# Optimization experiments

Measured on AMD Instinct MI355X. Metric: run time of the kernel, lower is better.

The kernel has to match this reference:

```python
import jax, jax.numpy as jnp
import numpy as np

N, D, RDIM, R, L = 512, 768, 100, 8, 2
EPS = 1e-5


def _ln(x, g, b):
    m = jnp.mean(x, axis=-1, keepdims=True)
    v = jnp.var(x, axis=-1, keepdims=True)
    return (x - m) * jax.lax.rsqrt(v + EPS) * g + b


def _conv2d(x, w, b):
    y = jax.lax.conv_general_dilated(x, w, (1, 1), 'SAME',
                                     dimension_numbers=('NCHW', 'OIHW', 'NCHW'))
    return y + b[None, :, None, None]


def setup_inputs() -> dict:
    key = jax.random.key(0)
    ks = jax.random.split(key, 10)
    s = 0.02
    inv = 1.0 / np.sqrt(D).astype(np.float32)
    return {
        'ents': jax.random.normal(ks[0], (N, D), jnp.float32),
        'R_local': jax.random.normal(ks[1], (L, RDIM, D, D), jnp.float32) * inv,
        'rel_mlp_w': jax.random.normal(ks[2], (R, RDIM), jnp.float32) * s,
        'rel_mlp_b': jnp.zeros((R,), jnp.float32),
        'conv1_w': jax.random.normal(ks[3], (L, 2 * RDIM, RDIM, 3, 3), jnp.float32) * s,
        'conv1_b': jnp.zeros((L, 2 * RDIM), jnp.float32),
        'conv2_w': jax.random.normal(ks[4], (L, RDIM, 2 * RDIM, 3, 3), jnp.float32) * s,
        'conv2_b': jnp.zeros((L, RDIM), jnp.float32),
        'posffn_ln_g': jnp.ones((L, RDIM), jnp.float32),
        'posffn_ln_b': jnp.zeros((L, RDIM), jnp.float32),
        'rel_ln_g': jnp.ones((L, RDIM), jnp.float32),
        'rel_ln_b': jnp.zeros((L, RDIM), jnp.float32),
        'mh_wf': jax.random.normal(ks[5], (L, R, D, D // R), jnp.float32) * inv,
        'mh_wb': jax.random.normal(ks[6], (L, R, D, D // R), jnp.float32) * inv,
        'mh_b': jnp.zeros((L, R, D // R), jnp.float32),
        'ent_mlp_w': jax.random.normal(ks[7], (L, D, D), jnp.float32) * inv,
        'ent_mlp_b': jnp.zeros((L, D), jnp.float32),
        'ent_ln_g': jnp.ones((L, D), jnp.float32),
        'ent_ln_b': jnp.zeros((L, D), jnp.float32),
    }


def reference(ents, R_local, rel_mlp_w, rel_mlp_b, conv1_w, conv1_b, conv2_w, conv2_b,
              posffn_ln_g, posffn_ln_b, rel_ln_g, rel_ln_b, mh_wf, mh_wb, mh_b,
              ent_mlp_w, ent_mlp_b, ent_ln_g, ent_ln_b):
    # Eval mode: dropout and dropedge are identity.
    prev_rels = None
    I = jnp.eye(N, dtype=ents.dtype)
    for l in range(L):
        residual = ents
        # ReRescal: rel[i, j, r] = e_i^T R_r e_j, then ReLU  -> [N, N, RDIM]
        t = jnp.einsum('id,rde->ire', ents, R_local[l])
        rel_embs = jax.nn.relu(jnp.einsum('ire,je->ijr', t, ents))
        if prev_rels is not None:
            rel_embs = _ln(rel_embs + prev_rels, rel_ln_g[l], rel_ln_b[l])
        # posFFN2d: 3x3 conv FFN over the NxN relation grid + residual layernorm
        res = rel_embs
        h = rel_embs.transpose(2, 0, 1)[None]  # [1, RDIM, N, N]
        h = jax.nn.relu(_conv2d(h, conv1_w[l], conv1_b[l]))
        h = _conv2d(h, conv2_w[l], conv2_b[l])[0].transpose(1, 2, 0)
        rel_embs = _ln(h + res, posffn_ln_g[l], posffn_ln_b[l])
        # relation logits -> softmax over relation axis -> [R, N, N] adjacency
        iap = jnp.einsum('ijd,rd->rij', rel_embs, rel_mlp_w) + rel_mlp_b[:, None, None]
        A = jax.nn.softmax(iap, axis=0)
        # Laplace smoothing: D^-1/2 (A + I) D^-1/2
        A_hat = A + I[None]
        dis = jax.lax.rsqrt(jnp.sum(A_hat, axis=2))
        dis = jnp.where(jnp.isinf(dis), 0.0, dis)
        A = dis[:, :, None] * A_hat * dis[:, None, :]
        # multi-head directed GCN (single layer, arch=[])
        hf = jnp.einsum('nd,rdo->rno', ents, mh_wf[l])
        hb = jnp.einsum('nd,rdo->rno', ents, mh_wb[l])
        out = (jnp.einsum('rmn,rno->rmo', A, hf)
               + jnp.einsum('rnm,rno->rmo', A, hb)
               + mh_b[l][:, None, :])
        out = jax.nn.relu(out)  # [R, N, D//R]
        e = out.transpose(1, 0, 2).reshape(N, D)
        # ent_mlp (single Linear) + residual layernorm
        e = jnp.einsum('nd,od->no', e, ent_mlp_w[l]) + ent_mlp_b[l]
        ents = _ln(e + residual, ent_ln_g[l], ent_ln_b[l])
        prev_rels = rel_embs
    rels = jnp.einsum('ijd,rd->ijr', prev_rels, rel_mlp_w) + rel_mlp_b
    return (ents, rels)
```

## Files before the change

kernel.cpp:

```cpp
#include <hip/hip_runtime.h>
#include <hip/hip_bf16.h>


static constexpr long NNpix = 512L * 512L;

typedef __attribute__((ext_vector_type(8))) short short8v;
typedef __attribute__((ext_vector_type(4))) float f32x4;

__device__ inline float bf2f(short s) {
    unsigned u = ((unsigned)(unsigned short)s) << 16;
    float f; __builtin_memcpy(&f, &u, 4);
    return f;
}
__device__ inline short f2bf(float f) {
    unsigned u; __builtin_memcpy(&u, &f, 4);
    u += 0x7fff + ((u >> 16) & 1);
    return (short)(u >> 16);
}
__device__ inline void gload_lds16(const short* g, short* l) {
    __builtin_amdgcn_global_load_lds(
        (const __attribute__((address_space(1))) unsigned int*)g,
        (__attribute__((address_space(3))) unsigned int*)l, 16, 0, 0);
}

template <bool RELU>
__global__ __launch_bounds__(256) void bgemm_xyt(
    const short* __restrict__ X, long sX,
    const short* __restrict__ Y, long sY,
    short* __restrict__ D, long sD,
    int M, int N, int K)
{
    X += (long)blockIdx.z * sX;
    Y += (long)blockIdx.z * sY;
    D += (long)blockIdx.z * sD;

    __shared__ short Xs[128 * 32];
    __shared__ short Ys[128 * 32];

    const int tid = threadIdx.x, wv = tid >> 6, ln = tid & 63;
    const int wr = wv >> 1, wc = wv & 1;
    const int m0 = blockIdx.y * 128, n0 = blockIdx.x * 128;

    f32x4 acc[4][4] = {};

    const int srow = ln >> 2;
    const int sk8 = ln & 3;
    const int fr = ln & 15, fk = (ln >> 4) * 8;

    for (int k0 = 0; k0 < K; k0 += 32) {
#pragma unroll
        for (int i = wv; i < 8; i += 4) {
            gload_lds16(X + (long)(m0 + i * 16 + srow) * K + k0 + sk8 * 8,
                        Xs + i * 512);
            gload_lds16(Y + (long)(n0 + i * 16 + srow) * K + k0 + sk8 * 8,
                        Ys + i * 512);
        }
        __syncthreads();
        short8v a[4], b[4];
#pragma unroll
        for (int mi = 0; mi < 4; ++mi)
            a[mi] = *(const short8v*)(Xs + (wr * 64 + mi * 16 + fr) * 32 + fk);
#pragma unroll
        for (int ni = 0; ni < 4; ++ni)
            b[ni] = *(const short8v*)(Ys + (wc * 64 + ni * 16 + fr) * 32 + fk);
#pragma unroll
        for (int mi = 0; mi < 4; ++mi)
#pragma unroll
            for (int ni = 0; ni < 4; ++ni)
                acc[mi][ni] = __builtin_amdgcn_mfma_f32_16x16x32_bf16(
                    a[mi], b[ni], acc[mi][ni], 0, 0, 0);
        __syncthreads();
    }

    const int fv = (ln >> 4) * 4;
#pragma unroll
    for (int mi = 0; mi < 4; ++mi)
#pragma unroll
        for (int ni = 0; ni < 4; ++ni)
#pragma unroll
            for (int v = 0; v < 4; ++v) {
                const int row = m0 + wr * 64 + mi * 16 + fv + v;
                const int col = n0 + wc * 64 + ni * 16 + fr;
                float x = acc[mi][ni][v];
                if (RELU) x = fmaxf(x, 0.f);
                D[(long)row * N + col] = f2bf(x);
            }
}

__global__ __launch_bounds__(256) void bgemm_bias_f32(
    const short* __restrict__ X,
    const short* __restrict__ Y,
    float* __restrict__ D,
    const float* __restrict__ bias,
    int M, int N, int K)
{
    __shared__ short Xs[128 * 32];
    __shared__ short Ys[128 * 32];

    const int tid = threadIdx.x, wv = tid >> 6, ln = tid & 63;
    const int wr = wv >> 1, wc = wv & 1;
    const int m0 = blockIdx.y * 128, n0 = blockIdx.x * 128;

    f32x4 acc[4][4] = {};

    const int srow = ln >> 2;
    const int sk8 = ln & 3;
    const int fr = ln & 15, fk = (ln >> 4) * 8;

    for (int k0 = 0; k0 < K; k0 += 32) {
#pragma unroll
        for (int i = wv; i < 8; i += 4) {
            gload_lds16(X + (long)(m0 + i * 16 + srow) * K + k0 + sk8 * 8,
                        Xs + i * 512);
            gload_lds16(Y + (long)(n0 + i * 16 + srow) * K + k0 + sk8 * 8,
                        Ys + i * 512);
        }
        __syncthreads();
        short8v a[4], b[4];
#pragma unroll
        for (int mi = 0; mi < 4; ++mi)
            a[mi] = *(const short8v*)(Xs + (wr * 64 + mi * 16 + fr) * 32 + fk);
#pragma unroll
        for (int ni = 0; ni < 4; ++ni)
            b[ni] = *(const short8v*)(Ys + (wc * 64 + ni * 16 + fr) * 32 + fk);
#pragma unroll
        for (int mi = 0; mi < 4; ++mi)
#pragma unroll
            for (int ni = 0; ni < 4; ++ni)
                acc[mi][ni] = __builtin_amdgcn_mfma_f32_16x16x32_bf16(
                    a[mi], b[ni], acc[mi][ni], 0, 0, 0);
        __syncthreads();
    }

    const int fv = (ln >> 4) * 4;
#pragma unroll
    for (int mi = 0; mi < 4; ++mi)
#pragma unroll
        for (int ni = 0; ni < 4; ++ni)
#pragma unroll
            for (int v = 0; v < 4; ++v) {
                const int row = m0 + wr * 64 + mi * 16 + fv + v;
                const int col = n0 + wc * 64 + ni * 16 + fr;
                D[(long)row * N + col] = acc[mi][ni][v] + bias[col];
            }
}

template <int CINP, int CINW, int COUT, int OUTP, bool RELU>
__global__ __launch_bounds__(256) void conv_gemm(
    const short* __restrict__ img,
    const short* __restrict__ wflat,
    const float* __restrict__ bias,
    short* __restrict__ out)
{
    constexpr int NCH = CINW / 32;
    constexpr int KW = 9 * CINW;

    __shared__ short Xs[144 * 32];
    __shared__ short Ys[3 * 128 * 32];

    const int tid = threadIdx.x, wv = tid >> 6, ln = tid & 63;
    const int wr = wv >> 1, wc = wv & 1;
    const int bx = blockIdx.x;
    const int bsw = (bx & 7) * ((int)gridDim.x >> 3) + (bx >> 3);
    const int m0 = bsw * 128;
    const int n0 = blockIdx.y * 128;

    f32x4 acc[4][4] = {};

    const int srow = ln >> 2;
    const int sk8 = ln & 3;
    const int fr = ln & 15, fk = (ln >> 4) * 8;

    for (int ky = 0; ky < 3; ++ky) {
        const int slab0 = m0 + (ky - 1) * 512 - 1;
        for (int cc = 0; cc < NCH; ++cc) {
            const int ci0 = cc * 32;
#pragma unroll
            for (int i = wv; i < 9; i += 4) {
                int rpx = slab0 + i * 16 + srow;
                rpx = rpx < 0 ? 0 : (rpx > (int)NNpix - 1 ? (int)NNpix - 1 : rpx);
                gload_lds16(img + (long)rpx * CINP + ci0 + sk8 * 8,
                            Xs + i * 512);
            }
#pragma unroll
            for (int kx = 0; kx < 3; ++kx) {
                const int wbase = (ky * 3 + kx) * CINW;
#pragma unroll
                for (int i = wv; i < 8; i += 4)
                    gload_lds16(wflat + (long)(n0 + i * 16 + srow) * KW + wbase + ci0 + sk8 * 8,
                                Ys + kx * 4096 + i * 512);
            }
            __syncthreads();
#pragma unroll
            for (int kx = 0; kx < 3; ++kx) {
                short8v a[4], b[4];
#pragma unroll
                for (int mi = 0; mi < 4; ++mi)
                    a[mi] = *(const short8v*)(Xs + (wr * 64 + mi * 16 + fr + kx) * 32 + fk);
#pragma unroll
                for (int ni = 0; ni < 4; ++ni)
                    b[ni] = *(const short8v*)(Ys + kx * 4096 + (wc * 64 + ni * 16 + fr) * 32 + fk);
#pragma unroll
                for (int mi = 0; mi < 4; ++mi)
#pragma unroll
                    for (int ni = 0; ni < 4; ++ni)
                        acc[mi][ni] = __builtin_amdgcn_mfma_f32_16x16x32_bf16(
                            a[mi], b[ni], acc[mi][ni], 0, 0, 0);
            }
            __syncthreads();
        }
    }

    const int fv = (ln >> 4) * 4;
#pragma unroll
    for (int mi = 0; mi < 4; ++mi)
#pragma unroll
        for (int ni = 0; ni < 4; ++ni)
#pragma unroll
            for (int v = 0; v < 4; ++v) {
                const int px = m0 + wr * 64 + mi * 16 + fv + v;
                const int co = n0 + wc * 64 + ni * 16 + fr;
                if (co < COUT) {
                    float x = acc[mi][ni][v] + bias[co];
                    if (RELU) x = fmaxf(x, 0.f);
                    out[(long)px * OUTP + co] = f2bf(x);
                } else if (co < OUTP) {
                    out[(long)px * OUTP + co] = 0;
                }
            }
}

template <int CINP, int CINW>
__global__ __launch_bounds__(256) void edge_gather(
    const short* __restrict__ img, short* __restrict__ EP)
{
    constexpr int KW = 9 * CINW;
    const int e = blockIdx.x;
    int y, x;
    bool real = true;
    if (e < 512)       { y = 0;   x = e; }
    else if (e < 1024) { y = 511; x = e - 512; }
    else if (e < 1534) { x = 0;   y = 1 + (e - 1024); }
    else if (e < 2044) { x = 511; y = 1 + (e - 1534); }
    else               { y = 0; x = 0; real = false; }

    const int tid = threadIdx.x;
    for (int idx = tid; idx < KW / 8; idx += 256) {
        const int tap = idx / (CINW / 8);
        const int c = (idx - tap * (CINW / 8)) * 8;
        short8v v = {0, 0, 0, 0, 0, 0, 0, 0};
        if (real && c < CINP) {
            const int yy = y + tap / 3 - 1, xx = x + tap % 3 - 1;
            if ((unsigned)yy < 512u && (unsigned)xx < 512u)
                v = *(const short8v*)(img + ((long)yy * 512 + xx) * CINP + c);
        }
        *(short8v*)(EP + (long)e * KW + idx * 8) = v;
    }
}

template <int COUT, int OUTP, bool RELU>
__global__ __launch_bounds__(256) void conv_edge_gemm(
    const short* __restrict__ EP,
    const short* __restrict__ wflat,
    const float* __restrict__ bias,
    short* __restrict__ out, int K)
{
    __shared__ short Xs[128 * 32];
    __shared__ short Ys[128 * 32];

    const int tid = threadIdx.x, wv = tid >> 6, ln = tid & 63;
    const int wr = wv >> 1, wc = wv & 1;
    const int m0 = blockIdx.x * 128, n0 = blockIdx.y * 128;

    f32x4 acc[4][4] = {};

    const int srow = ln >> 2;
    const int sk8 = ln & 3;
    const int fr = ln & 15, fk = (ln >> 4) * 8;

    for (int k0 = 0; k0 < K; k0 += 32) {
#pragma unroll
        for (int i = wv; i < 8; i += 4) {
            gload_lds16(EP + (long)(m0 + i * 16 + srow) * K + k0 + sk8 * 8,
                        Xs + i * 512);
            gload_lds16(wflat + (long)(n0 + i * 16 + srow) * K + k0 + sk8 * 8,
                        Ys + i * 512);
        }
        __syncthreads();
        short8v a[4], b[4];
#pragma unroll
        for (int mi = 0; mi < 4; ++mi)
            a[mi] = *(const short8v*)(Xs + (wr * 64 + mi * 16 + fr) * 32 + fk);
#pragma unroll
        for (int ni = 0; ni < 4; ++ni)
            b[ni] = *(const short8v*)(Ys + (wc * 64 + ni * 16 + fr) * 32 + fk);
#pragma unroll
        for (int mi = 0; mi < 4; ++mi)
#pragma unroll
            for (int ni = 0; ni < 4; ++ni)
                acc[mi][ni] = __builtin_amdgcn_mfma_f32_16x16x32_bf16(
                    a[mi], b[ni], acc[mi][ni], 0, 0, 0);
        __syncthreads();
    }

    const int fv = (ln >> 4) * 4;
#pragma unroll
    for (int mi = 0; mi < 4; ++mi)
#pragma unroll
        for (int ni = 0; ni < 4; ++ni)
#pragma unroll
            for (int v = 0; v < 4; ++v) {
                const int e = m0 + wr * 64 + mi * 16 + fv + v;
                const int co = n0 + wc * 64 + ni * 16 + fr;
                if (e >= 2044 || co >= COUT) continue;
                int y, x;
                if (e < 512)       { y = 0;   x = e; }
                else if (e < 1024) { y = 511; x = e - 512; }
                else if (e < 1534) { x = 0;   y = 1 + (e - 1024); }
                else               { x = 511; y = 1 + (e - 1534); }
                float v2 = acc[mi][ni][v] + bias[co];
                if (RELU) v2 = fmaxf(v2, 0.f);
                out[((long)y * 512 + x) * OUTP + co] = f2bf(v2);
            }
}

__global__ __launch_bounds__(256) void r_transpose(
    const float* __restrict__ R, short* __restrict__ Rt)
{
    __shared__ float Ts[64][65];
    const int tid = threadIdx.x;
    const long base = (long)blockIdx.z * 589824;
    const int d0 = blockIdx.y * 64, e0 = blockIdx.x * 64;
    const int c = tid & 63, rbase = tid >> 6;
#pragma unroll
    for (int j = 0; j < 16; ++j) {
        const int r = rbase + j * 4;
        Ts[r][c] = R[base + (long)(d0 + r) * 768 + e0 + c];
    }
    __syncthreads();
#pragma unroll
    for (int j = 0; j < 16; ++j) {
        const int e = rbase + j * 4;
        Rt[base + (long)(e0 + e) * 768 + d0 + c] = f2bf(Ts[c][e]);
    }
}

__global__ __launch_bounds__(256) void wfb_transpose(
    const float* __restrict__ wf, const float* __restrict__ wb,
    short* __restrict__ dst)
{
    __shared__ float Ts[64][65];
    const int tid = threadIdx.x;
    const int z = blockIdx.z;
    const float* src = (z < 8) ? wf + (long)z * 73728 : wb + (long)(z - 8) * 73728;
    const int d0 = blockIdx.x * 64, o0 = blockIdx.y * 64;
    const int c = tid & 63, rbase = tid >> 6;
#pragma unroll
    for (int j = 0; j < 16; ++j) {
        const int r = rbase + j * 4;
        Ts[r][c] = (o0 + c < 96) ? src[(long)(d0 + r) * 96 + o0 + c] : 0.f;
    }
    __syncthreads();
#pragma unroll
    for (int j = 0; j < 16; ++j) {
        const int e = rbase + j * 4;
        dst[(long)z * 98304 + (long)(o0 + e) * 768 + d0 + c] = f2bf(Ts[c][e]);
    }
}

__global__ __launch_bounds__(256) void a_laplace_t(
    const float* __restrict__ Ahat, const float* __restrict__ psum,
    short* __restrict__ ABF, short* __restrict__ ABFT)
{
    __shared__ float Ts[64][65];
    const int tid = threadIdx.x;
    const int r8 = blockIdx.z;
    const long ra = (long)r8 * 262144;
    const int i0 = blockIdx.y * 64, j0 = blockIdx.x * 64;
    const int c = tid & 63, rbase = tid >> 6;
    const float sj = psum[r8 * 1024 + (j0 + c) * 2] + psum[r8 * 1024 + (j0 + c) * 2 + 1];
    const float dj = rsqrtf(sj);
#pragma unroll
    for (int j = 0; j < 16; ++j) {
        const int r = rbase + j * 4;
        const float si = psum[r8 * 1024 + (i0 + r) * 2] + psum[r8 * 1024 + (i0 + r) * 2 + 1];
        const float di = rsqrtf(si);
        const float v = Ahat[ra + (long)(i0 + r) * 512 + j0 + c] * di * dj;
        Ts[r][c] = v;
        ABF[ra + (long)(i0 + r) * 512 + j0 + c] = f2bf(v);
    }
    __syncthreads();
#pragma unroll
    for (int j = 0; j < 16; ++j) {
        const int e = rbase + j * 4;
        ABFT[ra + (long)(j0 + e) * 512 + i0 + c] = f2bf(Ts[c][e]);
    }
}

__global__ __launch_bounds__(256) void gcn_combine(
    const short* __restrict__ O1, const short* __restrict__ O2,
    const float* __restrict__ mhb, short* __restrict__ e)
{
    const int idx = blockIdx.x * 256 + threadIdx.x;
    const int m = idx / 768, c = idx - m * 768;
    const int r = c / 96, o = c - r * 96;
    const long oi = (long)r * 65536 + (long)m * 128 + o;
    float v = bf2f(O1[oi]) + bf2f(O2[oi]) + mhb[c];
    e[idx] = f2bf(fmaxf(v, 0.f));
}

__global__ __launch_bounds__(256) void rel_transpose(
    const short* __restrict__ relc, short* __restrict__ relp)
{
    __shared__ short Ts[64][40];
    const int tid = threadIdx.x;
    const long p0 = (long)blockIdx.x * 64;
    const int r0 = blockIdx.y * 32;
    {
        const int ch = tid >> 3, pxo = (tid & 7) * 8;
        short8v v = {0, 0, 0, 0, 0, 0, 0, 0};
        if (r0 + ch < 100)
            v = *(const short8v*)(relc + (long)(r0 + ch) * NNpix + p0 + pxo);
#pragma unroll
        for (int j = 0; j < 8; ++j) Ts[pxo + j][ch] = v[j];
    }
    __syncthreads();
    const int px = tid >> 2, k8 = (tid & 3) * 8;
    if (r0 + k8 < 112) {
        const short8v o = *(const short8v*)(&Ts[px][k8]);
        *(short8v*)(relp + (p0 + px) * 112 + r0 + k8) = o;
    }
}

__global__ __launch_bounds__(256) void conv_w_flat(
    const float* __restrict__ src, short* __restrict__ dst,
    int COUT, int CIN, int COUTP, int CINW)
{
    const int idx = blockIdx.x * 256 + threadIdx.x;
    const int KW = 9 * CINW;
    const int total = COUTP * KW;
    if (idx >= total) return;
    const int co = idx / KW;
    const int rem = idx - co * KW;
    const int tap = rem / CINW, ci = rem - tap * CINW;
    short v = 0;
    if (co < COUT && ci < CIN)
        v = f2bf(src[((long)co * CIN + ci) * 9 + tap]);
    dst[idx] = v;
}

__global__ __launch_bounds__(256) void f32_to_bf16k(
    const float* __restrict__ src, short* __restrict__ dst, long n)
{
    const long i = (long)blockIdx.x * 256 + threadIdx.x;
    if (i < n) dst[i] = f2bf(src[i]);
}

__global__ __launch_bounds__(256) void ln_pix(
    const short* __restrict__ x, const short* __restrict__ res,
    const float* __restrict__ g, const float* __restrict__ b,
    short* __restrict__ out)
{
    __shared__ float gs[100], bs[100];
    const int tid = threadIdx.x;
    if (tid < 100) { gs[tid] = g[tid]; bs[tid] = b[tid]; }
    __syncthreads();
    const long p = (long)blockIdx.x * 256 + tid;
    const short* xr = x + p * 112;
    const short* rr = res + p * 112;
    float v[104];
    float s = 0.f, ss = 0.f;
#pragma unroll
    for (int q = 0; q < 13; ++q) {
        const short8v xa = *(const short8v*)(xr + q * 8);
        const short8v ra = *(const short8v*)(rr + q * 8);
#pragma unroll
        for (int j = 0; j < 8; ++j) {
            const int idx = q * 8 + j;
            const float t = bf2f(xa[j]) + bf2f(ra[j]);
            if (idx < 100) { v[idx] = t; s += t; ss += t * t; }
        }
    }
    const float mean = s * 0.01f;
    const float var = ss * 0.01f - mean * mean;
    const float inv = rsqrtf(var + 1e-5f);
    short* orow = out + p * 112;
#pragma unroll
    for (int q = 0; q < 14; ++q) {
        short8v o;
#pragma unroll
        for (int j = 0; j < 8; ++j) {
            const int idx = q * 8 + j;
            o[j] = (idx < 100) ? f2bf((v[idx] - mean) * inv * gs[idx] + bs[idx])
                               : (short)0;
        }
        *(short8v*)(orow + q * 8) = o;
    }
}

__global__ __launch_bounds__(256) void rel_softmax_laplace(
    const short* __restrict__ relp,
    const float* __restrict__ w,
    const float* __restrict__ bvec,
    float* __restrict__ Ahat,
    float* __restrict__ psum)
{
    __shared__ float ws[800];
    __shared__ float wred[8][4];
    const int tid = threadIdx.x;
    for (int i = tid; i < 800; i += 256) ws[i] = w[i];
    __syncthreads();

    const int i = blockIdx.y;
    const int j = blockIdx.x * 256 + tid;
    const long p = (long)i * 512 + j;
    const short* row = relp + p * 112;

    float acc[8];
#pragma unroll
    for (int r8 = 0; r8 < 8; ++r8) acc[r8] = bvec[r8];
#pragma unroll
    for (int q = 0; q < 13; ++q) {
        const short8v v = *(const short8v*)(row + q * 8);
#pragma unroll
        for (int jj = 0; jj < 8; ++jj) {
            const int r = q * 8 + jj;
            if (r < 100) {
                const float x = bf2f(v[jj]);
#pragma unroll
                for (int r8 = 0; r8 < 8; ++r8)
                    acc[r8] = fmaf(x, ws[r8 * 100 + r], acc[r8]);
            }
        }
    }
    float m = acc[0];
#pragma unroll
    for (int r8 = 1; r8 < 8; ++r8) m = fmaxf(m, acc[r8]);
    float s = 0.f;
#pragma unroll
    for (int r8 = 0; r8 < 8; ++r8) { acc[r8] = expf(acc[r8] - m); s += acc[r8]; }
    const float inv = 1.f / s;
#pragma unroll
    for (int r8 = 0; r8 < 8; ++r8) {
        const float a = acc[r8] * inv + (i == j ? 1.f : 0.f);
        acc[r8] = a;
        Ahat[(long)r8 * NNpix + p] = a;
    }
    const int lane = tid & 63, wvv = tid >> 6;
#pragma unroll
    for (int r8 = 0; r8 < 8; ++r8) {
        float v = acc[r8];
        for (int off = 32; off > 0; off >>= 1) v += __shfl_down(v, off);
        if (lane == 0) wred[r8][wvv] = v;
    }
    __syncthreads();
    if (tid < 8) {
        const float v = wred[tid][0] + wred[tid][1] + wred[tid][2] + wred[tid][3];
        psum[tid * 1024 + i * 2 + blockIdx.x] = v;
    }
}

__global__ __launch_bounds__(256) void ln_row768(
    const float* __restrict__ x, const float* __restrict__ res,
    const float* __restrict__ g, const float* __restrict__ b,
    float* __restrict__ out)
{
    const int n = blockIdx.x;
    const int tid = threadIdx.x;
    float v[3];
    float s = 0.f, ss = 0.f;
#pragma unroll
    for (int i = 0; i < 3; ++i) {
        const int c = tid + 256 * i;
        v[i] = x[(long)n * 768 + c] + res[(long)n * 768 + c];
        s += v[i]; ss += v[i] * v[i];
    }
    const int lane = tid & 63, wv = tid >> 6;
    for (int off = 32; off > 0; off >>= 1) {
        s += __shfl_down(s, off);
        ss += __shfl_down(ss, off);
    }
    __shared__ float rs[4], rss[4];
    if (lane == 0) { rs[wv] = s; rss[wv] = ss; }
    __syncthreads();
    s = rs[0] + rs[1] + rs[2] + rs[3];
    ss = rss[0] + rss[1] + rss[2] + rss[3];
    const float mean = s * (1.f / 768.f);
    const float var = ss * (1.f / 768.f) - mean * mean;
    const float inv = rsqrtf(var + 1e-5f);
#pragma unroll
    for (int i = 0; i < 3; ++i) {
        const int c = tid + 256 * i;
        out[(long)n * 768 + c] = (v[i] - mean) * inv * g[c] + b[c];
    }
}

__global__ __launch_bounds__(256) void final_rels(
    const short* __restrict__ relp, const float* __restrict__ w,
    const float* __restrict__ bvec, float* __restrict__ out)
{
    __shared__ float ws[800];
    const int tid = threadIdx.x;
    for (int i = tid; i < 800; i += 256) ws[i] = w[i];
    __syncthreads();
    const long p = (long)blockIdx.x * 256 + tid;
    const short* row = relp + p * 112;
    float acc[8];
#pragma unroll
    for (int r8 = 0; r8 < 8; ++r8) acc[r8] = bvec[r8];
#pragma unroll
    for (int q = 0; q < 13; ++q) {
        const short8v v = *(const short8v*)(row + q * 8);
#pragma unroll
        for (int jj = 0; jj < 8; ++jj) {
            const int r = q * 8 + jj;
            if (r < 100) {
                const float x = bf2f(v[jj]);
#pragma unroll
                for (int r8 = 0; r8 < 8; ++r8)
                    acc[r8] = fmaf(x, ws[r8 * 100 + r], acc[r8]);
            }
        }
    }
#pragma unroll
    for (int r8 = 0; r8 < 8; ++r8) out[p * 8 + r8] = acc[r8];
}

__global__ __launch_bounds__(256) void copy_f32(
    const float* __restrict__ src, float* __restrict__ dst, long n)
{
    const long i = (long)blockIdx.x * 256 + threadIdx.x;
    if (i < n) dst[i] = src[i];
}

__global__ __launch_bounds__(256) void zero_f32(float* __restrict__ p, long n)
{
    const long i = (long)blockIdx.x * 256 + threadIdx.x;
    if (i < n) p[i] = 0.f;
}

extern "C" void kernel_launch(void* const* d_in, const int* in_sizes, int n_in,
                              void* d_out, int out_size, void* d_ws, size_t ws_size,
                              hipStream_t stream)
{
    (void)in_sizes; (void)n_in; (void)out_size; (void)ws_size;

    const float* ents_in   = (const float*)d_in[0];
    const float* R_local   = (const float*)d_in[1];
    const float* rel_mlp_w = (const float*)d_in[2];
    const float* rel_mlp_b = (const float*)d_in[3];
    const float* conv1_w   = (const float*)d_in[4];
    const float* conv1_b   = (const float*)d_in[5];
    const float* conv2_w   = (const float*)d_in[6];
    const float* conv2_b   = (const float*)d_in[7];
    const float* pffn_g    = (const float*)d_in[8];
    const float* pffn_b    = (const float*)d_in[9];
    const float* rln_g     = (const float*)d_in[10];
    const float* rln_b     = (const float*)d_in[11];
    const float* mh_wf     = (const float*)d_in[12];
    const float* mh_wb     = (const float*)d_in[13];
    const float* mh_b      = (const float*)d_in[14];
    const float* emlp_w    = (const float*)d_in[15];
    const float* emlp_b    = (const float*)d_in[16];
    const float* eln_g     = (const float*)d_in[17];
    const float* eln_b     = (const float*)d_in[18];
    float* out = (float*)d_out;

    char* base = (char*)d_ws;
    size_t off = 0;
    auto alloc = [&](size_t bytes) {
        char* p = base + off;
        off += (bytes + 1023) & ~(size_t)1023;
        return p;
    };
    char* U1 = alloc(117964800 + 4096);
    short* RTL = (short*)U1;
    short* H1T = (short*)U1;
    char* U2 = alloc(78643200 + 4096);
    short* TB  = (short*)U2;
    short* O2P = (short*)U2;
    short* RELC   = (short*)alloc(52428800 + 4096);
    short* RELP_A = (short*)alloc(58720256 + 4096);
    short* RELP_B = (short*)alloc(58720256 + 4096);
    short* W1P = (short*)alloc(294912 * 2);
    short* W2P = (short*)alloc(258048 * 2);
    short* EPB = (short*)alloc(2048L * 2016 * 2 + 4096);
    const size_t tail0 = off;
    short* EBF  = (short*)alloc(393216L * 2);
    float* ABUF = (float*)alloc(2097152L * 4);
    float* PSUM = (float*)alloc(8192L * 4);
    short* ABF  = (short*)alloc(2097152L * 2);
    short* ABFT = (short*)alloc(2097152L * 2);
    short* WFBT = (short*)alloc(1572864L * 2);
    short* HFBT = (short*)alloc(1048576L * 2);
    short* O1B  = (short*)alloc(524288L * 2);
    short* O2B  = (short*)alloc(524288L * 2);
    short* EB2  = (short*)alloc(393216L * 2);
    short* EWB  = (short*)alloc(589824L * 2);
    float* E2   = (float*)alloc(393216L * 4);
    float* ENTS0 = (float*)alloc(393216L * 4);
    float* ENTS1 = (float*)alloc(393216L * 4);
    float* ENTS2 = (float*)alloc(393216L * 4);
    const long tailN = (long)((off - tail0) / 4);
    (void)O2B;

    zero_f32<<<(int)((tailN + 255) / 256), 256, 0, stream>>>(
        (float*)(base + tail0), tailN);
    copy_f32<<<1536, 256, 0, stream>>>(ents_in, ENTS0, 393216);

    for (int l = 0; l < 2; ++l) {
        short* RELP_cur = (l == 0) ? RELP_A : RELP_B;
        const float* ents_cur = (l == 0) ? ENTS0 : ENTS1;
        float* ents_next = (l == 0) ? ENTS1 : ENTS2;

        f32_to_bf16k<<<1536, 256, 0, stream>>>(ents_cur, EBF, 393216);

        r_transpose<<<dim3(12, 12, 100), 256, 0, stream>>>(
            R_local + (long)l * 58982400, RTL);

        bgemm_xyt<false><<<dim3(6, 4, 100), 256, 0, stream>>>(
            EBF, 0, RTL, 589824L, TB, 393216L, 512, 768, 768);
        bgemm_xyt<true><<<dim3(4, 4, 100), 256, 0, stream>>>(
            TB, 393216L, EBF, 0, RELC, 262144L, 512, 512, 768);
        rel_transpose<<<dim3(4096, 4), 256, 0, stream>>>(RELC, RELP_cur);
        if (l > 0)
            ln_pix<<<1024, 256, 0, stream>>>(RELP_cur, RELP_A,
                rln_g + l * 100, rln_b + l * 100, RELP_cur);

        conv_w_flat<<<1152, 256, 0, stream>>>(
            conv1_w + (long)l * 180000, W1P, 200, 100, 256, 128);
        conv_w_flat<<<1008, 256, 0, stream>>>(
            conv2_w + (long)l * 180000, W2P, 100, 200, 128, 224);

        conv_gemm<112, 128, 200, 208, true><<<dim3(2048, 2), 256, 0, stream>>>(
            RELP_cur, W1P, conv1_b + l * 200, H1T);
        edge_gather<112, 128><<<2048, 256, 0, stream>>>(RELP_cur, EPB);
        conv_edge_gemm<200, 208, true><<<dim3(16, 2), 256, 0, stream>>>(
            EPB, W1P, conv1_b + l * 200, H1T, 1152);

        conv_gemm<208, 224, 100, 112, false><<<dim3(2048, 1), 256, 0, stream>>>(
            H1T, W2P, conv2_b + l * 100, O2P);
        edge_gather<208, 224><<<2048, 256, 0, stream>>>(H1T, EPB);
        conv_edge_gemm<100, 112, false><<<dim3(16, 1), 256, 0, stream>>>(
            EPB, W2P, conv2_b + l * 100, O2P, 2016);

        ln_pix<<<1024, 256, 0, stream>>>(O2P, RELP_cur,
            pffn_g + l * 100, pffn_b + l * 100, RELP_cur);

        rel_softmax_laplace<<<dim3(2, 512), 256, 0, stream>>>(
            RELP_cur, rel_mlp_w, rel_mlp_b, ABUF, PSUM);
        a_laplace_t<<<dim3(8, 8, 8), 256, 0, stream>>>(ABUF, PSUM, ABF, ABFT);

        wfb_transpose<<<dim3(12, 2, 16), 256, 0, stream>>>(
            mh_wf + (long)l * 589824, mh_wb + (long)l * 589824, WFBT);
        bgemm_xyt<false><<<dim3(4, 1, 16), 256, 0, stream>>>(
            WFBT, 98304L, EBF, 0, HFBT, 65536L, 128, 512, 768);
        bgemm_xyt<false><<<dim3(1, 4, 16), 256, 0, stream>>>(
            ABF, 262144L, HFBT, 65536L, O1B, 65536L, 512, 128, 512);
        gcn_combine<<<1536, 256, 0, stream>>>(O1B, O1B + 8L * 65536,
                                              mh_b + l * 768, EB2);

        f32_to_bf16k<<<2304, 256, 0, stream>>>(
            emlp_w + (long)l * 589824, EWB, 589824);
        bgemm_bias_f32<<<dim3(6, 4), 256, 0, stream>>>(
            EB2, EWB, E2, emlp_b + l * 768, 512, 768, 768);
        ln_row768<<<512, 256, 0, stream>>>(E2, ents_cur,
            eln_g + l * 768, eln_b + l * 768, ents_next);
    }

    copy_f32<<<1536, 256, 0, stream>>>(ENTS2, out, 393216);
    final_rels<<<1024, 256, 0, stream>>>(RELP_B, rel_mlp_w, rel_mlp_b, out + 393216);
}
```

Before: 1.836 ms.

## Remap GEMM blocks across XCDs and store unnormalized adjacency in bf16

Adds a block-index remap to the two bf16 GEMM kernels so that consecutive linear block IDs, which the hardware spreads round-robin over the eight XCDs, are regrouped and each XCD works on a contiguous range of tiles. This is meant to improve L2 reuse of shared operand tiles. Separately, the softmax+identity adjacency buffer Ahat is now written and read as bf16 instead of fp32, halving that intermediate's traffic. The risk is a small precision loss before the Laplace normalisation, since row sums are still computed from the fp32 values.

```diff
diff --git a/kernel.cpp b/kernel.cpp
--- a/kernel.cpp
+++ b/kernel.cpp
@@ -21,6 +21,19 @@
     __builtin_amdgcn_global_load_lds(
         (const __attribute__((address_space(1))) unsigned int*)g,
         (__attribute__((address_space(3))) unsigned int*)l, 16, 0, 0);
+}
+
+__device__ inline void xcd_block3(int& bx, int& by, int& bz) {
+    const long gx = gridDim.x, gy = gridDim.y;
+    const long total = gx * gy * (long)gridDim.z;
+    long lin = blockIdx.x + gx * (blockIdx.y + gy * (long)blockIdx.z);
+    if ((total & 7) == 0)
+        lin = (lin & 7) * (total >> 3) + (lin >> 3);
+    const long gxy = gx * gy;
+    bz = (int)(lin / gxy);
+    const int rem = (int)(lin - (long)bz * gxy);
+    by = rem / (int)gx;
+    bx = rem - by * (int)gx;
 }
 
 template <bool RELU>
@@ -30,16 +43,18 @@
     short* __restrict__ D, long sD,
     int M, int N, int K)
 {
-    X += (long)blockIdx.z * sX;
-    Y += (long)blockIdx.z * sY;
-    D += (long)blockIdx.z * sD;
+    int bx, by, bz;
+    xcd_block3(bx, by, bz);
+    X += (long)bz * sX;
+    Y += (long)bz * sY;
+    D += (long)bz * sD;
 
     __shared__ short Xs[128 * 32];
     __shared__ short Ys[128 * 32];
 
     const int tid = threadIdx.x, wv = tid >> 6, ln = tid & 63;
     const int wr = wv >> 1, wc = wv & 1;
-    const int m0 = blockIdx.y * 128, n0 = blockIdx.x * 128;
+    const int m0 = by * 128, n0 = bx * 128;
 
     f32x4 acc[4][4] = {};
 
@@ -94,12 +109,16 @@
     const float* __restrict__ bias,
     int M, int N, int K)
 {
+    int bx, by, bz;
+    xcd_block3(bx, by, bz);
+    (void)bz;
+
     __shared__ short Xs[128 * 32];
     __shared__ short Ys[128 * 32];
 
     const int tid = threadIdx.x, wv = tid >> 6, ln = tid & 63;
     const int wr = wv >> 1, wc = wv & 1;
-    const int m0 = blockIdx.y * 128, n0 = blockIdx.x * 128;
+    const int m0 = by * 128, n0 = bx * 128;
 
     f32x4 acc[4][4] = {};
 
@@ -369,7 +388,7 @@
 }
 
 __global__ __launch_bounds__(256) void a_laplace_t(
-    const float* __restrict__ Ahat, const float* __restrict__ psum,
+    const short* __restrict__ Ahat, const float* __restrict__ psum,
     short* __restrict__ ABF, short* __restrict__ ABFT)
 {
     __shared__ float Ts[64][65];
@@ -385,7 +404,7 @@
         const int r = rbase + j * 4;
         const float si = psum[r8 * 1024 + (i0 + r) * 2] + psum[r8 * 1024 + (i0 + r) * 2 + 1];
         const float di = rsqrtf(si);
-        const float v = Ahat[ra + (long)(i0 + r) * 512 + j0 + c] * di * dj;
+        const float v = bf2f(Ahat[ra + (long)(i0 + r) * 512 + j0 + c]) * di * dj;
         Ts[r][c] = v;
         ABF[ra + (long)(i0 + r) * 512 + j0 + c] = f2bf(v);
     }
@@ -502,7 +521,7 @@
     const short* __restrict__ relp,
     const float* __restrict__ w,
     const float* __restrict__ bvec,
-    float* __restrict__ Ahat,
+    short* __restrict__ Ahat,
     float* __restrict__ psum)
 {
     __shared__ float ws[800];
@@ -544,7 +563,7 @@
     for (int r8 = 0; r8 < 8; ++r8) {
         const float a = acc[r8] * inv + (i == j ? 1.f : 0.f);
         acc[r8] = a;
-        Ahat[(long)r8 * NNpix + p] = a;
+        Ahat[(long)r8 * NNpix + p] = f2bf(a);
     }
     const int lane = tid & 63, wvv = tid >> 6;
 #pragma unroll
@@ -687,7 +706,7 @@
     short* EPB = (short*)alloc(2048L * 2016 * 2 + 4096);
     const size_t tail0 = off;
     short* EBF  = (short*)alloc(393216L * 2);
-    float* ABUF = (float*)alloc(2097152L * 4);
+    short* ABUF = (short*)alloc(2097152L * 2);
     float* PSUM = (float*)alloc(8192L * 4);
     short* ABF  = (short*)alloc(2097152L * 2);
     short* ABFT = (short*)alloc(2097152L * 2);
```

Result: no change. 1.820 ms (-0.9%).
